# Kernel tuning notes

Hardware: AMD Instinct MI355X
Metric: run time of the kernel (lower is better)

## Reference

```python
import jax, jax.numpy as jnp
import numpy as np

# LAB normalization constants (Zhang et al. colorization convention used in this repo)
L_CENT, L_NORM, AB_NORM = 50.0, 100.0, 110.0
_RGB2XYZ = np.array([[0.412453, 0.357580, 0.180423],
                     [0.212671, 0.715160, 0.072169],
                     [0.019334, 0.119193, 0.950227]], dtype=np.float32)
_XYZ_WHITE = np.array([0.95047, 1.0, 1.08883], dtype=np.float32)


def rgb2lab(rgb):
    """rgb: (B,3,H,W) in [-0.5,0.5] -> normalized LAB (B,3,H,W)."""
    rgb01 = rgb + 0.5  # [0,1]
    # sRGB gamma expansion (safe-where for grad stability)
    m = rgb01 > 0.04045
    rgb_safe = jnp.where(m, rgb01, 1.0)
    lin = jnp.where(m, ((rgb_safe + 0.055) / 1.055) ** 2.4, rgb01 / 12.92)
    xyz = jnp.einsum('ij,bjhw->bihw', jnp.asarray(_RGB2XYZ), lin)
    xyz = xyz / jnp.asarray(_XYZ_WHITE)[None, :, None, None]
    m2 = xyz > 0.008856
    xyz_safe = jnp.where(m2, xyz, 1.0)
    f = jnp.where(m2, xyz_safe ** (1.0 / 3.0), 7.787 * xyz + 16.0 / 116.0)
    L = 116.0 * f[:, 1] - 16.0
    a = 500.0 * (f[:, 0] - f[:, 1])
    b = 200.0 * (f[:, 1] - f[:, 2])
    return jnp.stack([(L - L_CENT) / L_NORM, a / AB_NORM, b / AB_NORM], axis=1)


def setup_inputs() -> dict:
    key = jax.random.key(0)
    k0, k1, k2, k3 = jax.random.split(key, 4)
    B, C, H, W, F = 2, 3, 64, 64, 64
    rgb0 = jax.random.uniform(k0, (B, C, H, W), dtype=jnp.float32) - 0.5
    rgb1 = jax.random.uniform(k1, (B, C, H, W), dtype=jnp.float32) - 0.5
    feat0 = jax.random.normal(k2, (B, F, H, W), dtype=jnp.float32)
    feat1 = jax.random.normal(k3, (B, F, H, W), dtype=jnp.float32)
    return {"rgb0": rgb0, "rgb1": rgb1, "feat0": feat0, "feat1": feat1}


def reference(rgb0, rgb1, feat0, feat1):
    l1_coeff, huber_coeff = 1.0, 1.0  # hyp.col2D_l1_coeff / hyp.col2D_huber_coeff
    B, C, H, W = rgb0.shape
    F = feat0.shape[1]
    N = H * W
    lab0 = rgb2lab(rgb0)
    lab1 = rgb2lab(rgb1)
    f0 = feat0.reshape(B, F, N)
    f1 = feat1.reshape(B, F, N)
    corr = jnp.einsum('bfn,bfm->bnm', f0, f1) / 0.07  # (B,N,N)
    att = jax.nn.softmax(corr, axis=2)
    lab1_flat = lab1.reshape(B, C, N)
    # broadcast-multiply-sum in the original == attention @ labels (same math)
    lab0_e = jnp.einsum('bnm,bcm->bcn', att, lab1_flat).reshape(B, C, H, W)
    diff = lab0_e - lab0
    l1_loss = jnp.mean(jnp.sum(jnp.abs(diff), axis=1, keepdims=True))
    ad = jnp.abs(diff)
    huber = jnp.where(ad < 1.0, 0.5 * ad * ad, ad - 0.5)  # SmoothL1, beta=1
    huber_loss = jnp.mean(jnp.sum(huber, axis=1, keepdims=True))
    total_loss = l1_coeff * l1_loss + huber_coeff * huber_loss
    return total_loss
```

## Files before the change

### kernel.cpp

```cpp
#include <hip/hip_runtime.h>
#include <math.h>

#define NPIX   4096
#define FDIM   64
#define BATCH  2
#define SPLIT  16
#define CHUNK  (NPIX / SPLIT)
#define NTILE  (CHUNK / 16)
#define BLKN   256

typedef __attribute__((ext_vector_type(8))) short short8;
typedef __attribute__((ext_vector_type(4))) float floatx4;

__device__ __forceinline__ float exp2f_(float x) { return __builtin_amdgcn_exp2f(x); }

__device__ __forceinline__ short f2bf(float x) {
    union { float f; unsigned u; } c; c.f = x;
    unsigned r = (c.u + 0x7FFFu + ((c.u >> 16) & 1u)) >> 16;
    return (short)r;
}

__device__ __forceinline__ float gamma_expand(float u) {
    return u > 0.04045f ? powf((u + 0.055f) * (1.0f / 1.055f), 2.4f)
                        : u * (1.0f / 12.92f);
}
__device__ __forceinline__ float lab_f(float t) {
    return t > 0.008856f ? cbrtf(t) : 7.787f * t + (16.0f / 116.0f);
}

__global__ __launch_bounds__(256) void prep_kernel(
    const float* __restrict__ rgb0, const float* __restrict__ rgb1,
    const float* __restrict__ feat0, const float* __restrict__ feat1,
    float* __restrict__ lab0, float* __restrict__ lab1,
    short* __restrict__ f0t, short* __restrict__ f1t,
    float* __restrict__ out)
{
    int bid = blockIdx.x;
    int tid = threadIdx.x;

    if (bid < 256) {
        __shared__ short Tsm[64 * 72];
        int pair = bid >> 6;
        int tensor = pair >> 1;
        int bb = pair & 1;
        int n0 = (bid & 63) * 64;
        const float* src = (tensor ? feat1 : feat0) + (size_t)bb * FDIM * NPIX;
        short* dst = (tensor ? f1t : f0t) + (size_t)bb * NPIX * FDIM;
        float scale = tensor ? 1.0f : (1.442695040888963f / 0.07f);

        int f = tid >> 2;
        int slot = tid & 3;
        #pragma unroll
        for (int i = 0; i < 4; ++i) {
            int col4 = slot * 4 + i;
            int noff = col4 * 4;
            float4 v = *(const float4*)&src[(size_t)f * NPIX + n0 + noff];
            Tsm[(noff + 0) * 72 + f] = f2bf(v.x * scale);
            Tsm[(noff + 1) * 72 + f] = f2bf(v.y * scale);
            Tsm[(noff + 2) * 72 + f] = f2bf(v.z * scale);
            Tsm[(noff + 3) * 72 + f] = f2bf(v.w * scale);
        }
        __syncthreads();
        #pragma unroll
        for (int i = 0; i < 2; ++i) {
            int idx = i * 256 + tid;
            int row = idx >> 3, ch = idx & 7;
            *(short8*)&dst[(size_t)(n0 + row) * FDIM + ch * 8] =
                *(const short8*)&Tsm[row * 72 + ch * 8];
        }
        return;
    }

    if (bid == 256 && tid == 0) out[0] = 0.0f;

    int gid = (bid - 256) * 256 + tid;
    int img = gid / (BATCH * NPIX);
    int rem = gid - img * (BATCH * NPIX);
    int b = rem / NPIX;
    int n = rem - b * NPIX;
    const float* rgb = img ? rgb1 : rgb0;
    float* lab = img ? lab1 : lab0;

    size_t i0 = (size_t)(b * 3 + 0) * NPIX + n;
    size_t i1 = (size_t)(b * 3 + 1) * NPIX + n;
    size_t i2 = (size_t)(b * 3 + 2) * NPIX + n;

    float r = gamma_expand(rgb[i0] + 0.5f);
    float g = gamma_expand(rgb[i1] + 0.5f);
    float bl = gamma_expand(rgb[i2] + 0.5f);

    float X = (0.412453f * r + 0.357580f * g + 0.180423f * bl) * (1.0f / 0.95047f);
    float Y = (0.212671f * r + 0.715160f * g + 0.072169f * bl);
    float Z = (0.019334f * r + 0.119193f * g + 0.950227f * bl) * (1.0f / 1.08883f);

    float fx = lab_f(X), fy = lab_f(Y), fz = lab_f(Z);
    float L = 116.0f * fy - 16.0f;
    float a = 500.0f * (fx - fy);
    float bb2 = 200.0f * (fy - fz);

    lab[i0] = (L - 50.0f) * (1.0f / 100.0f);
    lab[i1] = a * (1.0f / 110.0f);
    lab[i2] = bb2 * (1.0f / 110.0f);
}

__global__ __launch_bounds__(256, 2) void attn_kernel(
    const short* __restrict__ f0t, const short* __restrict__ f1t,
    const float* __restrict__ lab1ws, float* __restrict__ partials)
{
    __shared__ float Lt[3 * CHUNK];

    int bid = blockIdx.x;
    int rowblk = bid & 15;
    int chunk = (bid >> 4) & (SPLIT - 1);
    int b = bid >> 8;
    int tid = threadIdx.x;
    int w = tid >> 6;
    int l = tid & 63;
    int c = l & 15;
    int q = l >> 4;

    int n_base = rowblk * BLKN + w * 64;
    int m_base = chunk * CHUNK;

    if (tid < 192) {
        int cc = tid >> 6;
        int m4 = tid & 63;
        *(float4*)&Lt[cc * CHUNK + m4 * 4] =
            *(const float4*)&lab1ws[(size_t)(b * 3 + cc) * NPIX + m_base + m4 * 4];
    }

    short8 ya[4], yb[4];
    #pragma unroll
    for (int g = 0; g < 4; ++g) {
        const short8* yp = (const short8*)(f0t +
            ((size_t)b * NPIX + n_base + g * 16 + c) * FDIM + q * 8);
        ya[g] = yp[0];
        yb[g] = yp[4];
    }

    const short8* xbase = (const short8*)(f1t + ((size_t)b * NPIX + m_base + c) * FDIM + q * 8);

    short8 xa_r[4], xb_r[4];
    #pragma unroll
    for (int i = 0; i < 4; ++i) {
        xa_r[i] = xbase[(size_t)i * 128];
        xb_r[i] = xbase[(size_t)i * 128 + 4];
    }

    __syncthreads();

    float ms[4], sum[4], aA[4], aB[4], aC[4];
    #pragma unroll
    for (int g = 0; g < 4; ++g) {
        ms[g] = -INFINITY; sum[g] = 0.0f;
        aA[g] = 0.0f; aB[g] = 0.0f; aC[g] = 0.0f;
    }

    for (int tb = 0; tb < NTILE; tb += 4) {
        #pragma unroll
        for (int i = 0; i < 4; ++i) {
            int t = tb + i;

            floatx4 z = (floatx4)(0.0f);
            floatx4 acc[4];
            #pragma unroll
            for (int g = 0; g < 4; ++g) {
                acc[g] = __builtin_amdgcn_mfma_f32_16x16x32_bf16(xa_r[i], ya[g], z, 0, 0, 0);
                acc[g] = __builtin_amdgcn_mfma_f32_16x16x32_bf16(xb_r[i], yb[g], acc[g], 0, 0, 0);
            }

            if (t + 4 < NTILE) {
                xa_r[i] = xbase[(size_t)(t + 4) * 128];
                xb_r[i] = xbase[(size_t)(t + 4) * 128 + 4];
            }

            float4 lA = *(const float4*)&Lt[0 * CHUNK + t * 16 + q * 4];
            float4 lB = *(const float4*)&Lt[1 * CHUNK + t * 16 + q * 4];
            float4 lC = *(const float4*)&Lt[2 * CHUNK + t * 16 + q * 4];

            #pragma unroll
            for (int g = 0; g < 4; ++g) {
                float L0 = acc[g][0], L1 = acc[g][1], L2 = acc[g][2], L3 = acc[g][3];
                float tmax = fmaxf(fmaxf(L0, L1), fmaxf(L2, L3));
                float nm = fmaxf(ms[g], tmax);
                float sc = exp2f_(ms[g] - nm);
                float p0 = exp2f_(L0 - nm);
                float p1 = exp2f_(L1 - nm);
                float p2 = exp2f_(L2 - nm);
                float p3 = exp2f_(L3 - nm);
                sum[g] = sum[g] * sc + ((p0 + p1) + (p2 + p3));
                aA[g] = aA[g] * sc + ((p0 * lA.x + p1 * lA.y) + (p2 * lA.z + p3 * lA.w));
                aB[g] = aB[g] * sc + ((p0 * lB.x + p1 * lB.y) + (p2 * lB.z + p3 * lB.w));
                aC[g] = aC[g] * sc + ((p0 * lC.x + p1 * lC.y) + (p2 * lC.z + p3 * lC.w));
                ms[g] = nm;
            }
        }
    }

    #pragma unroll
    for (int mask = 16; mask <= 32; mask <<= 1) {
        #pragma unroll
        for (int g = 0; g < 4; ++g) {
            float om = __shfl_xor(ms[g], mask, 64);
            float os = __shfl_xor(sum[g], mask, 64);
            float oA = __shfl_xor(aA[g], mask, 64);
            float oB = __shfl_xor(aB[g], mask, 64);
            float oC = __shfl_xor(aC[g], mask, 64);
            float nm = fmaxf(ms[g], om);
            float w1 = exp2f_(ms[g] - nm);
            float w2 = exp2f_(om - nm);
            sum[g] = sum[g] * w1 + os * w2;
            aA[g] = aA[g] * w1 + oA * w2;
            aB[g] = aB[g] * w1 + oB * w2;
            aC[g] = aC[g] * w1 + oC * w2;
            ms[g] = nm;
        }
    }

    if (q == 0) {
        size_t pbase = (size_t)(b * SPLIT + chunk) * 5 * NPIX;
        #pragma unroll
        for (int g = 0; g < 4; ++g) {
            int n = n_base + g * 16 + c;
            partials[pbase + 0 * NPIX + n] = ms[g];
            partials[pbase + 1 * NPIX + n] = sum[g];
            partials[pbase + 2 * NPIX + n] = aA[g];
            partials[pbase + 3 * NPIX + n] = aB[g];
            partials[pbase + 4 * NPIX + n] = aC[g];
        }
    }
}

__global__ void loss_kernel(const float* __restrict__ partials,
                            const float* __restrict__ lab0ws,
                            float* __restrict__ out)
{
    int gid = blockIdx.x * blockDim.x + threadIdx.x;
    int b = gid >> 12;
    int n = gid & (NPIX - 1);

    float M = -INFINITY;
    #pragma unroll
    for (int ch = 0; ch < SPLIT; ++ch)
        M = fmaxf(M, partials[((size_t)(b * SPLIT + ch) * 5 + 0) * NPIX + n]);
    float S = 0.0f, A0 = 0.0f, A1 = 0.0f, A2 = 0.0f;
    #pragma unroll
    for (int ch = 0; ch < SPLIT; ++ch) {
        size_t base = (size_t)(b * SPLIT + ch) * 5 * NPIX + n;
        float w = exp2f_(partials[base + 0 * NPIX] - M);
        S  += partials[base + 1 * NPIX] * w;
        A0 += partials[base + 2 * NPIX] * w;
        A1 += partials[base + 3 * NPIX] * w;
        A2 += partials[base + 4 * NPIX] * w;
    }
    float inv_s = 1.0f / S;
    float d0 = A0 * inv_s - lab0ws[(size_t)(b * 3 + 0) * NPIX + n];
    float d1 = A1 * inv_s - lab0ws[(size_t)(b * 3 + 1) * NPIX + n];
    float d2 = A2 * inv_s - lab0ws[(size_t)(b * 3 + 2) * NPIX + n];

    float val = 0.0f;
    #pragma unroll
    for (int cc = 0; cc < 3; ++cc) {
        float d = (cc == 0) ? d0 : (cc == 1) ? d1 : d2;
        float ad = fabsf(d);
        float hub = (ad < 1.0f) ? 0.5f * ad * ad : ad - 0.5f;
        val += ad + hub;
    }

    #pragma unroll
    for (int off = 32; off > 0; off >>= 1)
        val += __shfl_down(val, off);

    __shared__ float wsum[4];
    int lane = threadIdx.x & 63;
    int wave = threadIdx.x >> 6;
    if (lane == 0) wsum[wave] = val;
    __syncthreads();
    if (threadIdx.x == 0) {
        float s = wsum[0] + wsum[1] + wsum[2] + wsum[3];
        atomicAdd(out, s * (1.0f / 8192.0f));
    }
}

extern "C" void kernel_launch(void* const* d_in, const int* in_sizes, int n_in,
                              void* d_out, int out_size, void* d_ws, size_t ws_size,
                              hipStream_t stream) {
    const float* rgb0  = (const float*)d_in[0];
    const float* rgb1  = (const float*)d_in[1];
    const float* feat0 = (const float*)d_in[2];
    const float* feat1 = (const float*)d_in[3];
    float* out = (float*)d_out;
    float* ws  = (float*)d_ws;

    float* lab0 = ws;
    float* lab1 = ws + 24576;
    float* partials = ws + 49152;
    short* f0t = (short*)(ws + 49152 + 655360);
    short* f1t = f0t + (size_t)BATCH * NPIX * FDIM;

    prep_kernel<<<320, 256, 0, stream>>>(rgb0, rgb1, feat0, feat1, lab0, lab1, f0t, f1t, out);

    int attn_grid = BATCH * SPLIT * (NPIX / BLKN);
    attn_kernel<<<attn_grid, 256, 0, stream>>>(f0t, f1t, lab1, partials);

    loss_kernel<<<(BATCH * NPIX) / 256, 256, 0, stream>>>(partials, lab0, out);
}
```

Measured before the change: 87.58 us.

## Stage key tile in padded LDS and split rows over eight waves

The attention kernel now loads the whole f1 chunk (256 keys x 64 bf16) into padded shared memory once per block. It no longer streams it from global memory in every wave with register prefetch. Blocks grow to 512 threads, and each wave handles 32 query rows instead of 64. This is meant to cut redundant global and L2 traffic for the keys and to raise occupancy and latency hiding. In exchange each wave does half as much MFMA work per shared-memory read, and the block adds about 36 KB of LDS.

```diff
diff --git a/kernel.cpp b/kernel.cpp
--- a/kernel.cpp
+++ b/kernel.cpp
@@ -8,6 +8,7 @@
 #define CHUNK  (NPIX / SPLIT)
 #define NTILE  (CHUNK / 16)
 #define BLKN   256
+#define PITCH  72
 
 typedef __attribute__((ext_vector_type(8))) short short8;
 typedef __attribute__((ext_vector_type(4))) float floatx4;
@@ -103,10 +104,11 @@
     lab[i2] = bb2 * (1.0f / 110.0f);
 }
 
-__global__ __launch_bounds__(256, 2) void attn_kernel(
+__global__ __launch_bounds__(512, 4) void attn_kernel(
     const short* __restrict__ f0t, const short* __restrict__ f1t,
     const float* __restrict__ lab1ws, float* __restrict__ partials)
 {
+    __shared__ short Xs[CHUNK * PITCH];
     __shared__ float Lt[3 * CHUNK];
 
     int bid = blockIdx.x;
@@ -114,12 +116,12 @@
     int chunk = (bid >> 4) & (SPLIT - 1);
     int b = bid >> 8;
     int tid = threadIdx.x;
-    int w = tid >> 6;
+    int wv = tid >> 6;
     int l = tid & 63;
     int c = l & 15;
     int q = l >> 4;
 
-    int n_base = rowblk * BLKN + w * 64;
+    int n_base = rowblk * BLKN + wv * 32;
     int m_base = chunk * CHUNK;
 
     if (tid < 192) {
@@ -129,78 +131,74 @@
             *(const float4*)&lab1ws[(size_t)(b * 3 + cc) * NPIX + m_base + m4 * 4];
     }
 
-    short8 ya[4], yb[4];
-    #pragma unroll
-    for (int g = 0; g < 4; ++g) {
+    {
+        const short8* src = (const short8*)(f1t + ((size_t)b * NPIX + m_base) * FDIM);
+        #pragma unroll
+        for (int i = 0; i < 4; ++i) {
+            int g = i * 512 + tid;
+            int m = g >> 3, kc = g & 7;
+            *(short8*)&Xs[m * PITCH + kc * 8] = src[g];
+        }
+    }
+
+    short8 ya[2], yb[2];
+    #pragma unroll
+    for (int g = 0; g < 2; ++g) {
         const short8* yp = (const short8*)(f0t +
             ((size_t)b * NPIX + n_base + g * 16 + c) * FDIM + q * 8);
         ya[g] = yp[0];
         yb[g] = yp[4];
     }
 
-    const short8* xbase = (const short8*)(f1t + ((size_t)b * NPIX + m_base + c) * FDIM + q * 8);
-
-    short8 xa_r[4], xb_r[4];
-    #pragma unroll
-    for (int i = 0; i < 4; ++i) {
-        xa_r[i] = xbase[(size_t)i * 128];
-        xb_r[i] = xbase[(size_t)i * 128 + 4];
-    }
-
     __syncthreads();
 
-    float ms[4], sum[4], aA[4], aB[4], aC[4];
-    #pragma unroll
-    for (int g = 0; g < 4; ++g) {
+    float ms[2], sum[2], aA[2], aB[2], aC[2];
+    #pragma unroll
+    for (int g = 0; g < 2; ++g) {
         ms[g] = -INFINITY; sum[g] = 0.0f;
         aA[g] = 0.0f; aB[g] = 0.0f; aC[g] = 0.0f;
     }
 
-    for (int tb = 0; tb < NTILE; tb += 4) {
-        #pragma unroll
-        for (int i = 0; i < 4; ++i) {
-            int t = tb + i;
-
-            floatx4 z = (floatx4)(0.0f);
-            floatx4 acc[4];
-            #pragma unroll
-            for (int g = 0; g < 4; ++g) {
-                acc[g] = __builtin_amdgcn_mfma_f32_16x16x32_bf16(xa_r[i], ya[g], z, 0, 0, 0);
-                acc[g] = __builtin_amdgcn_mfma_f32_16x16x32_bf16(xb_r[i], yb[g], acc[g], 0, 0, 0);
-            }
-
-            if (t + 4 < NTILE) {
-                xa_r[i] = xbase[(size_t)(t + 4) * 128];
-                xb_r[i] = xbase[(size_t)(t + 4) * 128 + 4];
-            }
-
-            float4 lA = *(const float4*)&Lt[0 * CHUNK + t * 16 + q * 4];
-            float4 lB = *(const float4*)&Lt[1 * CHUNK + t * 16 + q * 4];
-            float4 lC = *(const float4*)&Lt[2 * CHUNK + t * 16 + q * 4];
-
-            #pragma unroll
-            for (int g = 0; g < 4; ++g) {
-                float L0 = acc[g][0], L1 = acc[g][1], L2 = acc[g][2], L3 = acc[g][3];
-                float tmax = fmaxf(fmaxf(L0, L1), fmaxf(L2, L3));
-                float nm = fmaxf(ms[g], tmax);
-                float sc = exp2f_(ms[g] - nm);
-                float p0 = exp2f_(L0 - nm);
-                float p1 = exp2f_(L1 - nm);
-                float p2 = exp2f_(L2 - nm);
-                float p3 = exp2f_(L3 - nm);
-                sum[g] = sum[g] * sc + ((p0 + p1) + (p2 + p3));
-                aA[g] = aA[g] * sc + ((p0 * lA.x + p1 * lA.y) + (p2 * lA.z + p3 * lA.w));
-                aB[g] = aB[g] * sc + ((p0 * lB.x + p1 * lB.y) + (p2 * lB.z + p3 * lB.w));
-                aC[g] = aC[g] * sc + ((p0 * lC.x + p1 * lC.y) + (p2 * lC.z + p3 * lC.w));
-                ms[g] = nm;
-            }
+    #pragma unroll
+    for (int t = 0; t < NTILE; ++t) {
+        const short* xr = &Xs[(t * 16 + c) * PITCH + q * 8];
+        short8 xa = *(const short8*)xr;
+        short8 xb = *(const short8*)(xr + 32);
+
+        floatx4 z = (floatx4)(0.0f);
+        floatx4 acc[2];
+        #pragma unroll
+        for (int g = 0; g < 2; ++g) {
+            acc[g] = __builtin_amdgcn_mfma_f32_16x16x32_bf16(xa, ya[g], z, 0, 0, 0);
+            acc[g] = __builtin_amdgcn_mfma_f32_16x16x32_bf16(xb, yb[g], acc[g], 0, 0, 0);
+        }
+
+        float4 lA = *(const float4*)&Lt[0 * CHUNK + t * 16 + q * 4];
+        float4 lB = *(const float4*)&Lt[1 * CHUNK + t * 16 + q * 4];
+        float4 lC = *(const float4*)&Lt[2 * CHUNK + t * 16 + q * 4];
+
+        #pragma unroll
+        for (int g = 0; g < 2; ++g) {
+            float L0 = acc[g][0], L1 = acc[g][1], L2 = acc[g][2], L3 = acc[g][3];
+            float tmax = fmaxf(fmaxf(L0, L1), fmaxf(L2, L3));
+            float nm = fmaxf(ms[g], tmax);
+            float sc = exp2f_(ms[g] - nm);
+            float p0 = exp2f_(L0 - nm);
+            float p1 = exp2f_(L1 - nm);
+            float p2 = exp2f_(L2 - nm);
+            float p3 = exp2f_(L3 - nm);
+            sum[g] = sum[g] * sc + ((p0 + p1) + (p2 + p3));
+            aA[g] = aA[g] * sc + ((p0 * lA.x + p1 * lA.y) + (p2 * lA.z + p3 * lA.w));
+            aB[g] = aB[g] * sc + ((p0 * lB.x + p1 * lB.y) + (p2 * lB.z + p3 * lB.w));
+            aC[g] = aC[g] * sc + ((p0 * lC.x + p1 * lC.y) + (p2 * lC.z + p3 * lC.w));
+            ms[g] = nm;
         }
     }
 
     #pragma unroll
     for (int mask = 16; mask <= 32; mask <<= 1) {
         #pragma unroll
-        for (int g = 0; g < 4; ++g) {
+        for (int g = 0; g < 2; ++g) {
             float om = __shfl_xor(ms[g], mask, 64);
             float os = __shfl_xor(sum[g], mask, 64);
             float oA = __shfl_xor(aA[g], mask, 64);
@@ -220,7 +218,7 @@
     if (q == 0) {
         size_t pbase = (size_t)(b * SPLIT + chunk) * 5 * NPIX;
         #pragma unroll
-        for (int g = 0; g < 4; ++g) {
+        for (int g = 0; g < 2; ++g) {
             int n = n_base + g * 16 + c;
             partials[pbase + 0 * NPIX + n] = ms[g];
             partials[pbase + 1 * NPIX + n] = sum[g];
@@ -301,7 +299,7 @@
     prep_kernel<<<320, 256, 0, stream>>>(rgb0, rgb1, feat0, feat1, lab0, lab1, f0t, f1t, out);
 
     int attn_grid = BATCH * SPLIT * (NPIX / BLKN);
-    attn_kernel<<<attn_grid, 256, 0, stream>>>(f0t, f1t, lab1, partials);
+    attn_kernel<<<attn_grid, 512, 0, stream>>>(f0t, f1t, lab1, partials);
 
     loss_kernel<<<(BATCH * NPIX) / 256, 256, 0, stream>>>(partials, lab0, out);
 }
```

Result: faster. 83.06 us, median of 2 (-5.2%).
